# Performance work log

Hardware: AMD Instinct MI355X
Metric: run time of the kernel (lower is better)

The kernel has to match this reference:

```python
import jax, jax.numpy as jnp
import numpy as np

# ---- configuration (from init_kwargs / image geometry) ----
NUM_CLASSES = 10          # digit classes 1..10 (scores has K+1 cols, col 0 = background)
R = 500000                # total digit proposals for the image
T = 2048                  # topk_per_image: fixed-size survivor set for jit-friendly NMS
SCORE_T = 0.05            # digit_score_thresh
NMS_T = 0.5               # nms_thresh
IMG_W, IMG_H = 1920.0, 1080.0
CLS_OFFSET = IMG_W + IMG_H + 1.0  # batched_nms coordinate-offset trick (per-class NMS)


def setup_inputs() -> dict:
    key = jax.random.key(0)
    k1, k2, k3, k4 = jax.random.split(key, 4)
    # realistic boxes: uniform centers over the image, sizes in [10, 100] px
    cxcy = jax.random.uniform(k1, (R, 2)) * jnp.array([IMG_W, IMG_H], dtype=jnp.float32)
    wh = 10.0 + 90.0 * jax.random.uniform(k2, (R, 2))
    boxes = jnp.concatenate([cxcy - 0.5 * wh, cxcy + 0.5 * wh], axis=1)  # [R,4] x1y1x2y2
    # class probabilities over K+1 classes (col 0 = background)
    scores = jax.nn.softmax(jax.random.normal(k3, (R, NUM_CLASSES + 1)), axis=1)
    # per-box digit-center score (pred_digit_center_scores)
    center_scores = jax.random.uniform(k4, (R,))
    return {"boxes": boxes, "scores": scores, "center_scores": center_scores}


def _iou_matrix(b):
    # b: [T,4] in x1y1x2y2. Returns [T,T] pairwise IoU.
    area = jnp.clip(b[:, 2] - b[:, 0], 0.0) * jnp.clip(b[:, 3] - b[:, 1], 0.0)  # [T]
    lt = jnp.maximum(b[:, None, :2], b[None, :, :2])  # [T,T,2]
    rb = jnp.minimum(b[:, None, 2:], b[None, :, 2:])  # [T,T,2]
    wh = jnp.clip(rb - lt, 0.0)
    inter = wh[..., 0] * wh[..., 1]
    return inter / (area[:, None] + area[None, :] - inter + 1e-9)


def reference(boxes, scores, center_scores):
    # 1) drop background column, fuse with digit-center scores
    fg = scores[:, 1:] * center_scores[:, None]            # [R,K]
    # 2) clip boxes to image (Boxes.clip)
    clipped = jnp.stack([
        jnp.clip(boxes[:, 0], 0.0, IMG_W),
        jnp.clip(boxes[:, 1], 0.0, IMG_H),
        jnp.clip(boxes[:, 2], 0.0, IMG_W),
        jnp.clip(boxes[:, 3], 0.0, IMG_H),
    ], axis=1)                                             # [R,4]
    # 3) flatten (box, class) candidates and threshold (filter_mask = scores > thresh)
    flat = fg.reshape(-1)                                  # [R*K]
    masked = jnp.where(flat > SCORE_T, flat, -1.0)
    # 4) fixed-size pre-filter: top-T candidates by fused score
    vals, idx = jax.lax.top_k(masked, T)                   # sorted descending
    cand_boxes = clipped[idx // NUM_CLASSES]               # [T,4]
    cand_cls = idx % NUM_CLASSES                           # [T] (cls_id - 1)
    valid = vals > SCORE_T
    # 5) per-class batched NMS via coordinate-offset trick
    nms_boxes = cand_boxes + cand_cls.astype(cand_boxes.dtype)[:, None] * CLS_OFFSET
    iou = _iou_matrix(nms_boxes)                           # [T,T]
    rng = jnp.arange(T)
    def body(i, keep):
        sup = keep[i] & (iou[i] > NMS_T) & (rng > i)
        return keep & jnp.logical_not(sup)
    keep = jax.lax.fori_loop(0, T, body, valid)            # greedy NMS (inputs sorted by score)
    # 6) masked fixed-shape outputs: kept boxes + kept scores
    out_boxes = jnp.where(keep[:, None], cand_boxes, 0.0)
    out_scores = jnp.where(keep, vals, 0.0)
    return jnp.concatenate([out_boxes, out_scores[:, None]], axis=1)  # [T,5]
```

## Files before the change

### kernel.cpp

```cpp
#include <hip/hip_runtime.h>
#include <stdint.h>

typedef unsigned int u32;
typedef unsigned long long u64;

#define SCORE_THR 0.05f
#define NMS_THR   0.5f
#define TK        2048
#define CAP       4096
#define BASE14    ((int)(0x3D4CCCCDu >> 14))
#define MAGIC11   3123612579ull
#define NREP      8
#define PAIR_CAP  16384
#define SGRID     1024

#define WS_OFFS   0
#define WS_BINPOS 16384
#define WS_HDR    32768
#define WS_CBX    33024
#define WS_NBX    65792
#define WS_VALS   98560
#define WS_HREP   106752
#define WS_BUF    237824
#define WS_PAIRS  269824

__global__ void k_hist(const float* __restrict__ scores,
                       const float* __restrict__ center,
                       int R, u32* __restrict__ hrep) {
    __shared__ u32 h[4096];
    for (int t = threadIdx.x; t < 4096; t += blockDim.x) h[t] = 0;
    __syncthreads();
    int total_e = R * 11;
    int nq = total_e >> 2;
    int qpb = (nq + (int)gridDim.x - 1) / (int)gridDim.x;
    int start = (int)blockIdx.x * qpb;
    int end = start + qpb; if (end > nq) end = nq;
    int bd = (int)blockDim.x;
    for (int q = start + (int)threadIdx.x; q < end; q += 4 * bd) {
        int q1 = q + bd, q2 = q + 2 * bd, q3 = q + 3 * bd;
        float4 va, vb, vc, vd;
        bool ga = true, gb = q1 < end, gc = q2 < end, gd = q3 < end;
        va = ((const float4*)scores)[q];
        if (gb) vb = ((const float4*)scores)[q1];
        if (gc) vc = ((const float4*)scores)[q2];
        if (gd) vd = ((const float4*)scores)[q3];
#define HPROC(g, qq, v4)                                                   \
        if (g) {                                                           \
            float vv[4] = {v4.x, v4.y, v4.z, v4.w};                        \
            _Pragma("unroll")                                              \
            for (int j = 0; j < 4; j++) {                                  \
                u32 e2 = ((u32)(qq) << 2) + (u32)j;                        \
                u32 r = (u32)(((u64)e2 * MAGIC11) >> 35);                  \
                u32 c = e2 - r * 11u;                                      \
                if (c != 0u) {                                             \
                    float s = __fmul_rn(vv[j], center[r]);                 \
                    if (s > SCORE_THR) {                                   \
                        u32 key = __float_as_uint(s);                      \
                        int b = (int)(key >> 14) - BASE14;                 \
                        b = min(max(b, 0), 4095);                          \
                        atomicAdd(&h[b], 1u);                              \
                    }                                                      \
                }                                                          \
            }                                                              \
        }
        HPROC(ga, q, va) HPROC(gb, q1, vb) HPROC(gc, q2, vc) HPROC(gd, q3, vd)
#undef HPROC
    }
    if (blockIdx.x == 0 && threadIdx.x == 0) {
        for (int e2 = nq << 2; e2 < total_e; e2++) {
            u32 r = (u32)(((u64)(u32)e2 * MAGIC11) >> 35);
            u32 c = (u32)e2 - r * 11u;
            if (c != 0u) {
                float s = __fmul_rn(scores[e2], center[r]);
                if (s > SCORE_THR) {
                    u32 key = __float_as_uint(s);
                    int b = (int)(key >> 14) - BASE14;
                    b = min(max(b, 0), 4095);
                    atomicAdd(&h[b], 1u);
                }
            }
        }
    }
    __syncthreads();
    u32* hout = hrep + (size_t)(blockIdx.x & (NREP - 1)) * 4096;
    for (int t = threadIdx.x; t < 4096; t += blockDim.x)
        if (h[t]) atomicAdd(&hout[t], h[t]);
}

__global__ void k_scan(const u32* __restrict__ hrep, u32* __restrict__ offs,
                       u32* hdr) {
    int lane = threadIdx.x;
    int base = 4096 - 64 * (lane + 1);
    u32 v[64];
    u32 segsum = 0;
#pragma unroll
    for (int j = 0; j < 64; j++) {
        u32 s = 0;
#pragma unroll
        for (int i = 0; i < NREP; i++) s += hrep[i * 4096 + base + j];
        v[j] = s; segsum += s;
    }
    u32 incl = segsum;
    for (int off = 1; off < 64; off <<= 1) {
        u32 t = (u32)__shfl_up((int)incl, off);
        if (lane >= off) incl += t;
    }
    u32 excl = incl - segsum;
    u32 total = (u32)__shfl((int)incl, 63);
    u32 run = excl;
#pragma unroll
    for (int j = 63; j >= 0; j--) { offs[base + j] = run; run += v[j]; }
    if (lane == 0) hdr[6] = total;
    if (total < (u32)TK) {
        if (lane == 0) { hdr[3] = 0; hdr[5] = total; }
        return;
    }
    if ((excl < (u32)TK) && (incl >= (u32)TK)) {
        u32 cum = excl;
#pragma unroll
        for (int j = 63; j >= 0; j--) {
            u32 nc = cum + v[j];
            if (nc >= (u32)TK) { hdr[3] = (u32)(base + j); hdr[5] = nc; break; }
            cum = nc;
        }
    }
}

__global__ void k_collect(const float* __restrict__ scores,
                          const float* __restrict__ center,
                          int R, const u32* __restrict__ hdr,
                          const u32* __restrict__ offs, u32* __restrict__ binpos,
                          u64* __restrict__ buf) {
    u32 thr = hdr[3];
    int total_e = R * 11;
    int nq = total_e >> 2;
    int qpb = (nq + (int)gridDim.x - 1) / (int)gridDim.x;
    int start = (int)blockIdx.x * qpb;
    int end = start + qpb; if (end > nq) end = nq;
    int bd = (int)blockDim.x;
    for (int q = start + (int)threadIdx.x; q < end; q += 4 * bd) {
        int q1 = q + bd, q2 = q + 2 * bd, q3 = q + 3 * bd;
        float4 va, vb, vc, vd;
        bool ga = true, gb = q1 < end, gc = q2 < end, gd = q3 < end;
        va = ((const float4*)scores)[q];
        if (gb) vb = ((const float4*)scores)[q1];
        if (gc) vc = ((const float4*)scores)[q2];
        if (gd) vd = ((const float4*)scores)[q3];
#define CPROC(g, qq, v4)                                                   \
        if (g) {                                                           \
            float vv[4] = {v4.x, v4.y, v4.z, v4.w};                        \
            _Pragma("unroll")                                              \
            for (int j = 0; j < 4; j++) {                                  \
                u32 e2 = ((u32)(qq) << 2) + (u32)j;                        \
                u32 r = (u32)(((u64)e2 * MAGIC11) >> 35);                  \
                u32 c = e2 - r * 11u;                                      \
                if (c != 0u) {                                             \
                    float s = __fmul_rn(vv[j], center[r]);                 \
                    if (s > SCORE_THR) {                                   \
                        u32 key = __float_as_uint(s);                      \
                        int b = (int)(key >> 14) - BASE14;                 \
                        b = min(max(b, 0), 4095);                          \
                        if ((u32)b >= thr) {                               \
                            u32 slot = atomicAdd(&binpos[b], 1u);          \
                            u32 pos = offs[b] + slot;                      \
                            if (pos < CAP) {                               \
                                u32 idx = r * 10u + (c - 1u);              \
                                buf[pos] = ((u64)key << 32) | (u64)(~idx); \
                            }                                              \
                        }                                                  \
                    }                                                      \
                }                                                          \
            }                                                              \
        }
        CPROC(ga, q, va) CPROC(gb, q1, vb) CPROC(gc, q2, vc) CPROC(gd, q3, vd)
#undef CPROC
    }
    if (blockIdx.x == 0 && threadIdx.x == 0) {
        for (int e2 = nq << 2; e2 < total_e; e2++) {
            u32 r = (u32)(((u64)(u32)e2 * MAGIC11) >> 35);
            u32 c = (u32)e2 - r * 11u;
            if (c != 0u) {
                float s = __fmul_rn(scores[e2], center[r]);
                if (s > SCORE_THR) {
                    u32 key = __float_as_uint(s);
                    int b = (int)(key >> 14) - BASE14;
                    b = min(max(b, 0), 4095);
                    if ((u32)b >= thr) {
                        u32 slot = atomicAdd(&binpos[b], 1u);
                        u32 pos = offs[b] + slot;
                        if (pos < CAP) {
                            u32 idx = r * 10u + (c - 1u);
                            buf[pos] = ((u64)key << 32) | (u64)(~idx);
                        }
                    }
                }
            }
        }
    }
}

__global__ __launch_bounds__(1024) void k_rank(
        const float* __restrict__ boxes, const u32* __restrict__ offs,
        const u32* __restrict__ hdr, const u64* __restrict__ buf,
        float* __restrict__ cand_bx, float* __restrict__ nms_bx,
        float* __restrict__ vals) {
    __shared__ u64 kb[CAP];
    __shared__ u32 lo[4096];
    int tid = threadIdx.x;
    u32 n = hdr[5]; if (n > (u32)CAP) n = CAP;
    u32 total = hdr[6];
    for (int t = tid; t < CAP; t += 1024) kb[t] = (t < (int)n) ? buf[t] : 0ull;
    for (int t = tid; t < 4096; t += 1024) lo[t] = offs[t];
    __syncthreads();
    for (int i = tid; i < (int)n; i += 1024) {
        u64 x = kb[i];
        u32 key = (u32)(x >> 32);
        int b = (int)(key >> 14) - BASE14;
        b = min(max(b, 0), 4095);
        u32 start = lo[b];
        u32 end = (b > 0) ? lo[b - 1] : total;
        if (end > (u32)CAP) end = CAP;
        u32 rk = start;
        for (u32 j = start; j < end; j++) rk += (kb[j] > x) ? 1u : 0u;
        if (rk < (u32)TK) {
            u32 idx = ~(u32)x;
            u32 r = idx / 10u, cls = idx % 10u;
            const float* bp = boxes + (size_t)r * 4;
            float c0 = fminf(fmaxf(bp[0], 0.f), 1920.f);
            float c1 = fminf(fmaxf(bp[1], 0.f), 1080.f);
            float c2 = fminf(fmaxf(bp[2], 0.f), 1920.f);
            float c3 = fminf(fmaxf(bp[3], 0.f), 1080.f);
            float offv = __fmul_rn((float)cls, 3001.0f);
            cand_bx[rk * 4 + 0] = c0; cand_bx[rk * 4 + 1] = c1;
            cand_bx[rk * 4 + 2] = c2; cand_bx[rk * 4 + 3] = c3;
            nms_bx[rk * 4 + 0] = __fadd_rn(c0, offv);
            nms_bx[rk * 4 + 1] = __fadd_rn(c1, offv);
            nms_bx[rk * 4 + 2] = __fadd_rn(c2, offv);
            nms_bx[rk * 4 + 3] = __fadd_rn(c3, offv);
            vals[rk] = __uint_as_float(key);
        }
    }
}

__global__ void k_mask(const float* __restrict__ nms_bx, u32* __restrict__ hdr,
                       u32* __restrict__ pairs) {
    int colbase = blockIdx.x * 64, rowbase = blockIdx.y * 64;
    if (colbase + 63 <= rowbase) return;
    __shared__ float4 cb[64];
    __shared__ float ca[64];
    int tid = threadIdx.x;
    float4 c = ((const float4*)nms_bx)[colbase + tid];
    cb[tid] = c;
    ca[tid] = __fmul_rn(fmaxf(__fsub_rn(c.z, c.x), 0.f),
                        fmaxf(__fsub_rn(c.w, c.y), 0.f));
    int row = rowbase + tid;
    float4 rb = ((const float4*)nms_bx)[row];
    float rarea = __fmul_rn(fmaxf(__fsub_rn(rb.z, rb.x), 0.f),
                            fmaxf(__fsub_rn(rb.w, rb.y), 0.f));
    __syncthreads();
    for (int cc = 0; cc < 64; cc++) {
        int col = colbase + cc;
        if (col > row) {
            float4 cbv = cb[cc];
            float ltx = fmaxf(rb.x, cbv.x), lty = fmaxf(rb.y, cbv.y);
            float rbx = fminf(rb.z, cbv.z), rby = fminf(rb.w, cbv.w);
            float w = fmaxf(__fsub_rn(rbx, ltx), 0.f);
            float h = fmaxf(__fsub_rn(rby, lty), 0.f);
            float inter = __fmul_rn(w, h);
            float denom = __fadd_rn(__fsub_rn(__fadd_rn(rarea, ca[cc]), inter), 1e-9f);
            float iou = __fdiv_rn(inter, denom);
            if (iou > NMS_THR) {
                u32 p = atomicAdd(&hdr[8], 1u);
                if (p < PAIR_CAP)
                    pairs[p] = ((u32)row << 11) | (u32)col;
            }
        }
    }
}

__global__ __launch_bounds__(64) void k_final(
        const u32* __restrict__ pairs, const u32* __restrict__ hdr,
        const float* __restrict__ vals, const float* __restrict__ cand_bx,
        float* __restrict__ out) {
    __shared__ u32 sp[PAIR_CAP];
    __shared__ u32 cur[2048];
    int lane = threadIdx.x;
    u32 np = hdr[8]; if (np > (u32)PAIR_CAP) np = PAIR_CAP;
    const float4* vp = (const float4*)vals + (size_t)lane * 8;
    float4 vv[8];
#pragma unroll
    for (int j = 0; j < 8; j++) vv[j] = vp[j];
    u32 validw = 0;
#pragma unroll
    for (int j = 0; j < 8; j++) {
        validw |= (vv[j].x > SCORE_THR ? 1u : 0u) << (4 * j + 0);
        validw |= (vv[j].y > SCORE_THR ? 1u : 0u) << (4 * j + 1);
        validw |= (vv[j].z > SCORE_THR ? 1u : 0u) << (4 * j + 2);
        validw |= (vv[j].w > SCORE_THR ? 1u : 0u) << (4 * j + 3);
    }
    for (int t = lane; t < 2048; t += 64) cur[t] = 0;
    __syncthreads();
    for (u32 k = lane; k < np; k += 64) atomicAdd(&cur[pairs[k] >> 11], 1u);
    __syncthreads();
    u32 cnt[32];
    u32 seg = 0;
#pragma unroll
    for (int j = 0; j < 32; j++) { cnt[j] = cur[lane * 32 + j]; seg += cnt[j]; }
    u32 incl = seg;
    for (int off = 1; off < 64; off <<= 1) {
        u32 t = (u32)__shfl_up((int)incl, off);
        if (lane >= off) incl += t;
    }
    u32 run = incl - seg;
#pragma unroll
    for (int j = 0; j < 32; j++) { cur[lane * 32 + j] = run; run += cnt[j]; }
    __syncthreads();
    for (u32 k = lane; k < np; k += 64) {
        u32 p = pairs[k];
        u32 pos = atomicAdd(&cur[p >> 11], 1u);
        sp[pos] = p;
    }
    __syncthreads();
    u32 removed = 0;
    for (u32 k = 0; k < np; k++) {
        u32 p = sp[k];
        u32 row = p >> 11, col = p & 2047u;
        u32 aw = (u32)__shfl((int)(validw & ~removed), (int)(row >> 5));
        if ((aw >> (row & 31)) & 1u)
            if (lane == (int)(col >> 5)) removed |= 1u << (col & 31);
    }
    u32 keepw = validw & ~removed;
#pragma unroll
    for (int b = 0; b < 32; b++) {
        int i = lane * 32 + b;
        bool kp = (keepw >> b) & 1u;
        const float4 bx = ((const float4*)cand_bx)[i];
        float v = (b & 3) == 0 ? vv[b >> 2].x :
                  (b & 3) == 1 ? vv[b >> 2].y :
                  (b & 3) == 2 ? vv[b >> 2].z : vv[b >> 2].w;
        out[i * 5 + 0] = kp ? bx.x : 0.f;
        out[i * 5 + 1] = kp ? bx.y : 0.f;
        out[i * 5 + 2] = kp ? bx.z : 0.f;
        out[i * 5 + 3] = kp ? bx.w : 0.f;
        out[i * 5 + 4] = kp ? v : 0.f;
    }
}

extern "C" void kernel_launch(void* const* d_in, const int* in_sizes, int n_in,
                              void* d_out, int out_size, void* d_ws, size_t ws_size,
                              hipStream_t stream) {
    const float* boxes = (const float*)d_in[0];
    const float* scores = (const float*)d_in[1];
    const float* center = (const float*)d_in[2];
    float* out = (float*)d_out;
    int R = in_sizes[2];

    char* w = (char*)d_ws;
    u32* offs   = (u32*)(w + WS_OFFS);
    u32* binpos = (u32*)(w + WS_BINPOS);
    u32* hdr    = (u32*)(w + WS_HDR);
    float* cbx  = (float*)(w + WS_CBX);
    float* nbx  = (float*)(w + WS_NBX);
    float* vls  = (float*)(w + WS_VALS);
    u32* hrep   = (u32*)(w + WS_HREP);
    u64* buf    = (u64*)(w + WS_BUF);
    u32* pairs  = (u32*)(w + WS_PAIRS);

    hipMemsetAsync(w + WS_BINPOS, 0, WS_BUF - WS_BINPOS, stream);

    k_hist<<<SGRID, 256, 0, stream>>>(scores, center, R, hrep);
    k_scan<<<1, 64, 0, stream>>>(hrep, offs, hdr);
    k_collect<<<SGRID, 256, 0, stream>>>(scores, center, R, hdr, offs, binpos, buf);
    k_rank<<<1, 1024, 0, stream>>>(boxes, offs, hdr, buf, cbx, nbx, vls);
    k_mask<<<dim3(32, 32), 64, 0, stream>>>(nbx, hdr, pairs);
    k_final<<<1, 64, 0, stream>>>(pairs, hdr, vls, cbx, out);
}
```

Before: 141.2 us.

## Stash high-score candidates during histogram pass to skip collect rescan

The histogram kernel now also writes every candidate whose score key is at or above a fixed spill key (about 0.2) into a per-block shared-memory segment, then copies that segment to a global spill buffer. The collect kernel reads these small spill segments instead of rescanning the full scores array, whenever at least TK candidates were spilled and no segment overflowed. Otherwise it falls back to the original full scan. This removes a second full pass over scores and center. In exchange it adds shared atomics and spill writes in the histogram pass, and the fast path is correct only if the top-TK threshold bin lies above the spill key, which is not explicitly checked.

New measurement: 143.8 us. About the same (+1.8%).

```diff
diff --git a/kernel.cpp b/kernel.cpp
--- a/kernel.cpp
+++ b/kernel.cpp
@@ -9,10 +9,12 @@
 #define TK        2048
 #define CAP       4096
 #define BASE14    ((int)(0x3D4CCCCDu >> 14))
+#define SPILL_KEY 0x3E4CC000u
 #define MAGIC11   3123612579ull
 #define NREP      8
 #define PAIR_CAP  16384
 #define SGRID     1024
+#define SEGCAP    1024
 
 #define WS_OFFS   0
 #define WS_BINPOS 16384
@@ -23,12 +25,20 @@
 #define WS_HREP   106752
 #define WS_BUF    237824
 #define WS_PAIRS  269824
+#define WS_SCNT   335360
+#define WS_SPILL  339456
 
 __global__ void k_hist(const float* __restrict__ scores,
                        const float* __restrict__ center,
-                       int R, u32* __restrict__ hrep) {
+                       int R, u32* __restrict__ hrep,
+                       u64* __restrict__ spill, u32* __restrict__ scnt,
+                       u32* __restrict__ hdr) {
     __shared__ u32 h[4096];
-    for (int t = threadIdx.x; t < 4096; t += blockDim.x) h[t] = 0;
+    __shared__ u64 lseg[SEGCAP];
+    __shared__ u32 sc;
+    int tid = threadIdx.x;
+    for (int t = tid; t < 4096; t += blockDim.x) h[t] = 0;
+    if (tid == 0) sc = 0;
     __syncthreads();
     int total_e = R * 11;
     int nq = total_e >> 2;
@@ -36,7 +46,7 @@
     int start = (int)blockIdx.x * qpb;
     int end = start + qpb; if (end > nq) end = nq;
     int bd = (int)blockDim.x;
-    for (int q = start + (int)threadIdx.x; q < end; q += 4 * bd) {
+    for (int q = start + tid; q < end; q += 4 * bd) {
         int q1 = q + bd, q2 = q + 2 * bd, q3 = q + 3 * bd;
         float4 va, vb, vc, vd;
         bool ga = true, gb = q1 < end, gc = q2 < end, gd = q3 < end;
@@ -59,6 +69,12 @@
                         int b = (int)(key >> 14) - BASE14;                 \
                         b = min(max(b, 0), 4095);                          \
                         atomicAdd(&h[b], 1u);                              \
+                        if (key >= SPILL_KEY) {                            \
+                            u32 idx = r * 10u + (c - 1u);                  \
+                            u32 pos = atomicAdd(&sc, 1u);                  \
+                            if (pos < SEGCAP)                              \
+                                lseg[pos] = ((u64)key << 32) | (u64)(~idx);\
+                        }                                                  \
                     }                                                      \
                 }                                                          \
             }                                                              \
@@ -66,7 +82,7 @@
         HPROC(ga, q, va) HPROC(gb, q1, vb) HPROC(gc, q2, vc) HPROC(gd, q3, vd)
 #undef HPROC
     }
-    if (blockIdx.x == 0 && threadIdx.x == 0) {
+    if (blockIdx.x == 0 && tid == 0) {
         for (int e2 = nq << 2; e2 < total_e; e2++) {
             u32 r = (u32)(((u64)(u32)e2 * MAGIC11) >> 35);
             u32 c = (u32)e2 - r * 11u;
@@ -77,14 +93,28 @@
                     int b = (int)(key >> 14) - BASE14;
                     b = min(max(b, 0), 4095);
                     atomicAdd(&h[b], 1u);
+                    if (key >= SPILL_KEY) {
+                        u32 idx = r * 10u + (c - 1u);
+                        u32 pos = atomicAdd(&sc, 1u);
+                        if (pos < SEGCAP)
+                            lseg[pos] = ((u64)key << 32) | (u64)(~idx);
+                    }
                 }
             }
         }
     }
     __syncthreads();
+    u32 m = min(sc, (u32)SEGCAP);
+    u64* seg = spill + (size_t)blockIdx.x * SEGCAP;
+    for (u32 t = tid; t < m; t += blockDim.x) seg[t] = lseg[t];
     u32* hout = hrep + (size_t)(blockIdx.x & (NREP - 1)) * 4096;
-    for (int t = threadIdx.x; t < 4096; t += blockDim.x)
+    for (int t = tid; t < 4096; t += blockDim.x)
         if (h[t]) atomicAdd(&hout[t], h[t]);
+    if (tid == 0) {
+        scnt[blockIdx.x] = m;
+        atomicAdd(&hdr[12], m);
+        if (sc > (u32)SEGCAP) atomicOr(&hdr[13], 1u);
+    }
 }
 
 __global__ void k_scan(const u32* __restrict__ hrep, u32* __restrict__ offs,
@@ -127,18 +157,36 @@
 }
 
 __global__ void k_collect(const float* __restrict__ scores,
-                          const float* __restrict__ center,
-                          int R, const u32* __restrict__ hdr,
-                          const u32* __restrict__ offs, u32* __restrict__ binpos,
-                          u64* __restrict__ buf) {
+                          const float* __restrict__ center, int R,
+                          const u64* __restrict__ spill, const u32* __restrict__ scnt,
+                          const u32* __restrict__ hdr, const u32* __restrict__ offs,
+                          u32* __restrict__ binpos, u64* __restrict__ buf) {
     u32 thr = hdr[3];
+    bool happy = (hdr[12] >= (u32)TK) && (hdr[13] == 0u);
+    if (happy) {
+        u32 n = scnt[blockIdx.x];
+        const u64* seg = spill + (size_t)blockIdx.x * SEGCAP;
+        for (u32 i = threadIdx.x; i < n; i += blockDim.x) {
+            u64 v = seg[i];
+            u32 key = (u32)(v >> 32);
+            int b = (int)(key >> 14) - BASE14;
+            b = min(max(b, 0), 4095);
+            if ((u32)b >= thr) {
+                u32 slot = atomicAdd(&binpos[b], 1u);
+                u32 pos = offs[b] + slot;
+                if (pos < CAP) buf[pos] = v;
+            }
+        }
+        return;
+    }
     int total_e = R * 11;
     int nq = total_e >> 2;
     int qpb = (nq + (int)gridDim.x - 1) / (int)gridDim.x;
     int start = (int)blockIdx.x * qpb;
     int end = start + qpb; if (end > nq) end = nq;
     int bd = (int)blockDim.x;
-    for (int q = start + (int)threadIdx.x; q < end; q += 4 * bd) {
+    int tid = threadIdx.x;
+    for (int q = start + tid; q < end; q += 4 * bd) {
         int q1 = q + bd, q2 = q + 2 * bd, q3 = q + 3 * bd;
         float4 va, vb, vc, vd;
         bool ga = true, gb = q1 < end, gc = q2 < end, gd = q3 < end;
@@ -175,7 +223,7 @@
         CPROC(ga, q, va) CPROC(gb, q1, vb) CPROC(gc, q2, vc) CPROC(gd, q3, vd)
 #undef CPROC
     }
-    if (blockIdx.x == 0 && threadIdx.x == 0) {
+    if (blockIdx.x == 0 && tid == 0) {
         for (int e2 = nq << 2; e2 < total_e; e2++) {
             u32 r = (u32)(((u64)(u32)e2 * MAGIC11) >> 35);
             u32 c = (u32)e2 - r * 11u;
@@ -365,12 +413,15 @@
     u32* hrep   = (u32*)(w + WS_HREP);
     u64* buf    = (u64*)(w + WS_BUF);
     u32* pairs  = (u32*)(w + WS_PAIRS);
+    u32* scnt   = (u32*)(w + WS_SCNT);
+    u64* spill  = (u64*)(w + WS_SPILL);
 
     hipMemsetAsync(w + WS_BINPOS, 0, WS_BUF - WS_BINPOS, stream);
 
-    k_hist<<<SGRID, 256, 0, stream>>>(scores, center, R, hrep);
+    k_hist<<<SGRID, 256, 0, stream>>>(scores, center, R, hrep, spill, scnt, hdr);
     k_scan<<<1, 64, 0, stream>>>(hrep, offs, hdr);
-    k_collect<<<SGRID, 256, 0, stream>>>(scores, center, R, hdr, offs, binpos, buf);
+    k_collect<<<SGRID, 256, 0, stream>>>(scores, center, R, spill, scnt, hdr,
+                                         offs, binpos, buf);
     k_rank<<<1, 1024, 0, stream>>>(boxes, offs, hdr, buf, cbx, nbx, vls);
     k_mask<<<dim3(32, 32), 64, 0, stream>>>(nbx, hdr, pairs);
     k_final<<<1, 64, 0, stream>>>(pairs, hdr, vls, cbx, out);
```
